# Performance work log

Hardware: AMD Instinct MI355X
Metric: run time of the kernel (lower is better)

## Reference

```python
import jax, jax.numpy as jnp
import numpy as np
from jax import lax

N = 16384      # total nodes (NG graphs x PER nodes)
PER = 512      # nodes per graph
NG = 32        # number of graphs
E = 262144     # edges (avg degree 16)
NEG = jnp.float32(-1e30)


def gcn_conv(x, W, b, src, dst, em, n):
    # PyG GCNConv: h = xW; add *remaining* self-loops; symmetric norm; aggregate at dst; + bias
    h = x @ W
    w = em.astype(x.dtype)
    selfw = jax.ops.segment_sum(jnp.where((src == dst) & em, 1.0, 0.0), dst, num_segments=n)
    has_self = (selfw > 0).astype(x.dtype)
    deg = jax.ops.segment_sum(w, dst, num_segments=n) + (1.0 - has_self)
    dinv = lax.rsqrt(deg)
    norm = dinv[src] * dinv[dst] * w                      # [E]
    agg = jax.ops.segment_sum(norm[:, None] * h[src], dst, num_segments=n)
    return agg + ((1.0 - has_self) / deg)[:, None] * h + b


def edge_pool(x, src, dst, em, nvalid, Pw, Pb, n):
    # PyG EdgePooling with softmax edge scores, add_to_edge_score=0.1, eval-mode dropout (identity)
    e = src.shape[0]
    raw = (jnp.concatenate([x[src], x[dst]], axis=1) @ Pw)[:, 0] + Pb[0]
    # softmax over edges grouped by target node
    logits = jnp.where(em, raw, NEG)
    mx = jax.ops.segment_max(logits, dst, num_segments=n)
    ex = jnp.where(em, jnp.exp(raw - mx[dst]), 0.0)
    den = jax.ops.segment_sum(ex, dst, num_segments=n)
    score = jnp.where(em, ex / jnp.maximum(den[dst], 1e-16), 0.0) + 0.1
    # greedy sequential edge contraction in descending score order (matches PyG __merge_edges__)
    key = lax.stop_gradient(jnp.where(em, score, NEG))
    order = jnp.argsort(-key)

    def step(marked, sdm):
        s, d, mk = sdm
        ok = mk & ~marked[s] & ~marked[d]
        m1 = marked.at[s].set(marked[s] | ok)
        m2 = m1.at[d].set(m1[d] | ok)
        return m2, ok

    _, ch_sorted = lax.scan(step, ~nvalid, (src[order], dst[order], em[order]))
    chosen = jnp.zeros(e, bool).at[order].set(ch_sorted)

    rep = jnp.minimum(src, dst)
    oth = jnp.maximum(src, dst)
    SEN = n  # out-of-range index -> dropped scatter
    cluster = jnp.arange(n, dtype=src.dtype).at[jnp.where(chosen, oth, SEN)].set(rep, mode='drop')
    node_score = jnp.ones(n, x.dtype).at[jnp.where(chosen, rep, SEN)].set(score, mode='drop')
    absorbed = jnp.zeros(n, bool).at[jnp.where(chosen & (src != dst), oth, SEN)].set(True, mode='drop')
    new_valid = nvalid & ~absorbed
    # new_x[c] = (sum of x over cluster) * edge score (1 for unmatched nodes)
    new_x = jax.ops.segment_sum(x, cluster, num_segments=n) * node_score[:, None]
    new_x = new_x * new_valid[:, None].astype(x.dtype)
    # remap + coalesce edges (dedupe); padding kept via mask
    ns, nd = cluster[src], cluster[dst]
    ekey = jnp.where(em, ns * n + nd, n * n)
    eo = jnp.argsort(ekey)
    ks = ekey[eo]
    dup = jnp.concatenate([jnp.zeros(1, bool), ks[1:] == ks[:-1]])
    return new_x, ns[eo], nd[eo], (ks < n * n) & ~dup, new_valid


def _forward(x, W1, b1, W2, b2, W3, b3, P1w, P1b, P2w, P2b, P3w, P3b,
             L1w, L1b, L2w, L2b, L3w, L3b, edge_index, batch):
    n = x.shape[0]
    src, dst = edge_index[0], edge_index[1]
    em = jnp.ones(src.shape[0], bool)
    nv = jnp.ones(n, bool)
    h = gcn_conv(x, W1, b1, src, dst, em, n)
    h, src, dst, em, nv = edge_pool(h, src, dst, em, nv, P1w, P1b, n)
    h = jax.nn.relu(h)
    h = gcn_conv(h, W2, b2, src, dst, em, n)
    h, src, dst, em, nv = edge_pool(h, src, dst, em, nv, P2w, P2b, n)
    h = jax.nn.relu(h)
    h = gcn_conv(h, W3, b3, src, dst, em, n)
    h, src, dst, em, nv = edge_pool(h, src, dst, em, nv, P3w, P3b, n)
    h = jax.nn.relu(h)
    beff = jnp.where(nv, batch, NG)                       # invalid nodes -> dummy segment
    g = jax.ops.segment_max(h, beff, num_segments=NG + 1)[:NG]
    z = jax.nn.relu(g @ L1w + L1b)
    z = jax.nn.relu(z @ L2w + L2b)
    z = jax.nn.relu(z @ L3w + L3b)
    return jax.nn.softmax(z, axis=-1)


def _lin(k, fi, fo):
    w = jax.random.normal(k, (fi, fo), jnp.float32) * (1.0 / np.sqrt(fi))
    return w, jnp.zeros((fo,), jnp.float32)


def setup_inputs() -> dict:
    key = jax.random.key(0)
    ks = jax.random.split(key, 16)
    x = jax.random.normal(ks[0], (N, 107), jnp.float32)
    src = jax.random.randint(ks[1], (E,), 0, N, dtype=jnp.int32)
    dst = (src // PER) * PER + jax.random.randint(ks[2], (E,), 0, PER, dtype=jnp.int32)
    edge_index = jnp.stack([src, dst])
    batch = jnp.arange(N, dtype=jnp.int32) // PER
    W1, b1 = _lin(ks[3], 107, 200)
    W2, b2 = _lin(ks[4], 200, 400)
    W3, b3 = _lin(ks[5], 400, 600)
    P1w, P1b = _lin(ks[6], 400, 1)
    P2w, P2b = _lin(ks[7], 800, 1)
    P3w, P3b = _lin(ks[8], 1200, 1)
    L1w, L1b = _lin(ks[9], 600, 200)
    L2w, L2b = _lin(ks[10], 200, 20)
    L3w, L3b = _lin(ks[11], 20, 4)
    return dict(x=x, edge_index=edge_index, batch=batch,
                W1=W1, b1=b1, W2=W2, b2=b2, W3=W3, b3=b3,
                P1w=P1w, P1b=P1b, P2w=P2w, P2b=P2b, P3w=P3w, P3b=P3b,
                L1w=L1w, L1b=L1b, L2w=L2w, L2b=L2b, L3w=L3w, L3b=L3b)


def reference(x, edge_index, batch, W1, b1, W2, b2, W3, b3,
              P1w, P1b, P2w, P2b, P3w, P3b, L1w, L1b, L2w, L2b, L3w, L3b):
    return _forward(x, W1, b1, W2, b2, W3, b3, P1w, P1b, P2w, P2b, P3w, P3b,
                    L1w, L1b, L2w, L2b, L3w, L3b, edge_index, batch)
```

## Files before the change

### kernel.cpp

```cpp
#include <hip/hip_runtime.h>

#define NN 16384
#define PERG 512
#define NGR 32
#define NE 262144
#define GSEG 9216

typedef unsigned long long u64;

__device__ __forceinline__ unsigned encf(float f){
  unsigned u = __float_as_uint(f);
  return (u & 0x80000000u) ? ~u : (u | 0x80000000u);
}
__device__ __forceinline__ float decf(unsigned e){
  unsigned u = (e & 0x80000000u) ? (e ^ 0x80000000u) : ~e;
  return __uint_as_float(u);
}

__global__ void k_padx(const float* __restrict__ x, float* __restrict__ xp){
  int i = blockIdx.x*256 + threadIdx.x;
  if (i < NN*112){ int r = i/112, c = i-r*112; xp[i] = (c<107) ? x[r*107+c] : 0.f; }
}
__global__ void k_padw(const float* __restrict__ Wsrc, float* __restrict__ Wdst,
                       int Ksrc, int Kdst, int N){
  int i = blockIdx.x*256 + threadIdx.x;
  if (i < Kdst*N){ int r = i/N, c = i-r*N; Wdst[i] = (r<Ksrc) ? Wsrc[r*N+c] : 0.f; }
}

__global__ __launch_bounds__(256) void k_bucket(const int* __restrict__ ei, int* __restrict__ gcount,
    int* __restrict__ bsrc, int* __restrict__ bdst, int* __restrict__ bem, int* __restrict__ beid){
  __shared__ int cnt[NGR];
  __shared__ int base[NGR];
  int t = threadIdx.x;
  if (t < NGR) cnt[t] = 0;
  __syncthreads();
  int e = blockIdx.x*256 + t;
  int s=0,d=0,g=0,r=0;
  bool ok = (e < NE);
  if (ok){ s = ei[e]; d = ei[NE+e]; g = s >> 9; r = atomicAdd(&cnt[g],1); }
  __syncthreads();
  if (t < NGR) base[t] = atomicAdd(&gcount[t], cnt[t]);
  __syncthreads();
  if (ok){
    int pos = g*GSEG + base[g] + r;
    bsrc[pos]=s; bdst[pos]=d; bem[pos]=1; beid[pos]=e;
  }
}
__global__ void k_init_nodes(int* __restrict__ valid){
  int i = blockIdx.x*256 + threadIdx.x;
  if (i < NN) valid[i]=1;
}

__global__ __launch_bounds__(256) void k_mm(const float* __restrict__ A, const float* __restrict__ W,
                                            float* __restrict__ C, int KP, int N){
  __shared__ float As[16][132];
  __shared__ float Ws[16][68];
  int col0 = blockIdx.x*64, row0 = blockIdx.y*128;
  int t = threadIdx.x;
  int tx = t & 15, ty = t >> 4;
  int ar = t >> 1;
  int ak = (t & 1) * 8;
  int wk = t >> 4;
  int wn = (t & 15) * 4;
  int wc = col0 + wn;

  float acc[8][4];
#pragma unroll
  for (int i=0;i<8;i++)
#pragma unroll
    for (int j=0;j<4;j++) acc[i][j]=0.f;

  const float* Arow = A + (size_t)(row0+ar)*KP;

  for (int k0=0; k0<KP; k0+=16){
    float4 a0 = *(const float4*)&Arow[k0 + ak];
    float4 a1 = *(const float4*)&Arow[k0 + ak + 4];
    float4 w0;
    const float* wp = &W[(size_t)(k0+wk)*N + wc];
    if (wc+3 < N) w0 = *(const float4*)wp;
    else { w0.x=(wc<N)?wp[0]:0.f; w0.y=(wc+1<N)?wp[1]:0.f; w0.z=(wc+2<N)?wp[2]:0.f; w0.w=0.f; }
    __syncthreads();
    As[ak+0][ar]=a0.x; As[ak+1][ar]=a0.y; As[ak+2][ar]=a0.z; As[ak+3][ar]=a0.w;
    As[ak+4][ar]=a1.x; As[ak+5][ar]=a1.y; As[ak+6][ar]=a1.z; As[ak+7][ar]=a1.w;
    *(float4*)&Ws[wk][wn] = w0;
    __syncthreads();
#pragma unroll
    for (int kk=0;kk<16;kk++){
      float4 A0 = *(const float4*)&As[kk][ty*8];
      float4 A1 = *(const float4*)&As[kk][ty*8+4];
      float4 B0 = *(const float4*)&Ws[kk][tx*4];
      float a[8] = {A0.x,A0.y,A0.z,A0.w,A1.x,A1.y,A1.z,A1.w};
      float b[4] = {B0.x,B0.y,B0.z,B0.w};
#pragma unroll
      for (int i=0;i<8;i++)
#pragma unroll
        for (int j=0;j<4;j++) acc[i][j] += a[i]*b[j];
    }
  }

#pragma unroll
  for (int i=0;i<8;i++){
    int r = row0 + ty*8 + i;
    int cc = col0 + tx*4;
    if (cc+3 < N){
      float4 v = {acc[i][0],acc[i][1],acc[i][2],acc[i][3]};
      *(float4*)&C[(size_t)r*N+cc] = v;
    } else {
#pragma unroll
      for (int j=0;j<4;j++) if (cc+j<N) C[(size_t)r*N+cc+j] = acc[i][j];
    }
  }
}

__global__ __launch_bounds__(1024) void k_prep(const int* __restrict__ bsrc, const int* __restrict__ bdst,
    const int* __restrict__ bem, const int* __restrict__ gcount,
    int* __restrict__ row_s, int* __restrict__ row_e, int* __restrict__ elist,
    float* __restrict__ dinv, float* __restrict__ selfco){
  int g = blockIdx.x, t = threadIdx.x;
  __shared__ int cnt_l[PERG];
  __shared__ int scn[PERG];
  __shared__ int cur[PERG];
  __shared__ unsigned char hs_l[PERG];
  if (t<PERG){ cnt_l[t]=0; hs_l[t]=0; }
  __syncthreads();
  int nE = min(gcount[g], GSEG); int base = g*GSEG;
  for (int k=t;k<nE;k+=1024){
    if (bem[base+k]){
      int d = bdst[base+k]&511;
      atomicAdd(&cnt_l[d],1);
      if (bsrc[base+k]==bdst[base+k]) hs_l[d]=1;
    }
  }
  __syncthreads();
  if (t<PERG) scn[t]=cnt_l[t];
  __syncthreads();
  for (int off=1; off<PERG; off<<=1){
    int v = (t<PERG && t>=off) ? scn[t-off] : 0;
    __syncthreads();
    if (t<PERG) scn[t]+=v;
    __syncthreads();
  }
  if (t<PERG){
    int excl = scn[t]-cnt_l[t];
    row_s[g*PERG+t] = base+excl;
    row_e[g*PERG+t] = base+scn[t];
    cur[t] = excl;
    float deg = (float)cnt_l[t] + (hs_l[t]?0.f:1.f);
    dinv[g*PERG+t]   = rsqrtf(deg);
    selfco[g*PERG+t] = hs_l[t]?0.f:(1.f/deg);
  }
  __syncthreads();
  for (int k=t;k<nE;k+=1024){
    if (bem[base+k]){
      int d = bdst[base+k]&511;
      elist[base + atomicAdd(&cur[d],1)] = bsrc[base+k];
    }
  }
}

template<int FO>
__global__ __launch_bounds__(256) void k_aggab(const float* __restrict__ h, const int* __restrict__ row_s,
    const int* __restrict__ row_e, const int* __restrict__ elist,
    const float* __restrict__ dinv, const float* __restrict__ selfco, const float* __restrict__ bias,
    const float* __restrict__ Pw, float* __restrict__ y, float* __restrict__ aval, float* __restrict__ bval){
  constexpr int Q = (FO+63)/64;
  int lane = threadIdx.x & 63;
  int nblk = (blockIdx.x & 7)*512 + (blockIdx.x >> 3);
  int i = nblk*4 + (threadIdx.x>>6);
  float acc[Q];
#pragma unroll
  for (int q=0;q<Q;q++) acc[q]=0.f;
  int s0 = row_s[i], s1 = row_e[i];
  float di = dinv[i];
  for (int p=s0; p<s1; p++){
    int s = elist[p];
    float nr = di * dinv[s];
    const float* hrow = h + (size_t)s*FO;
#pragma unroll
    for (int q=0;q<Q;q++){ int c=lane+q*64; if (c<FO) acc[q] += nr*hrow[c]; }
  }
  float sc = selfco[i];
  const float* hi = h + (size_t)i*FO;
  float* yi = y + (size_t)i*FO;
  float sa=0.f, sb=0.f;
#pragma unroll
  for (int q=0;q<Q;q++){
    int c = lane+q*64;
    if (c<FO){
      float v = acc[q] + sc*hi[c] + bias[c];
      yi[c] = v;
      sa += v*Pw[c];
      sb += v*Pw[FO+c];
    }
  }
  for (int o=32;o;o>>=1){ sa += __shfl_xor(sa,o); sb += __shfl_xor(sb,o); }
  if (lane==0){ aval[i]=sa; bval[i]=sb; }
}

#define NEPT 9
__global__ __launch_bounds__(1024) void k_pool(const int* __restrict__ gcount,
    int* __restrict__ bsrc, int* __restrict__ bdst, int* __restrict__ bem, const int* __restrict__ beid,
    const float* __restrict__ aval, const float* __restrict__ bval, const float* __restrict__ Pb,
    float* __restrict__ nscore, int* __restrict__ partner, int* __restrict__ valid, int* __restrict__ table){
  extern __shared__ u64 dynL[];
  u64* list = dynL;
  unsigned* sdL = (unsigned*)(dynL + GSEG);
  __shared__ unsigned mx[PERG];
  __shared__ float den[PERG];
  __shared__ u64 best[PERG];
  __shared__ unsigned char marked[PERG];
  __shared__ unsigned short clus[PERG];
  __shared__ int cntA;
  int g = blockIdx.x, t = threadIdx.x;
  int nE = min(gcount[g], GSEG), base = g*GSEG;
  if (t<PERG){
    mx[t]=0u; den[t]=0.f; best[t]=0ull;
    marked[t] = valid[(g<<9)+t] ? 0 : 1;
    clus[t] = (unsigned short)t;
    nscore[(g<<9)+t] = 1.f;
    partner[(g<<9)+t] = -1;
  }
  if (t==0) cntA = 0;
  __syncthreads();

  int sL[NEPT], dL[NEPT];
  float rawv[NEPT];
  unsigned em = 0u;
#pragma unroll
  for (int j=0;j<NEPT;j++){
    sL[j]=0; dL[j]=0; rawv[j]=0.f;
    int k = t + j*1024;
    if (k < nE && bem[base+k]){
      sL[j] = bsrc[base+k]&511; dL[j] = bdst[base+k]&511;
      rawv[j] = aval[(g<<9)+sL[j]] + bval[(g<<9)+dL[j]] + Pb[0];
      em |= (1u<<j);
      atomicMax(&mx[dL[j]], encf(rawv[j]));
    }
  }
  __syncthreads();
  float exv[NEPT];
#pragma unroll
  for (int j=0;j<NEPT;j++){
    exv[j]=0.f;
    if (em & (1u<<j)){
      exv[j] = expf(rawv[j] - decf(mx[dL[j]]));
      atomicAdd(&den[dL[j]], exv[j]);
    }
  }
  __syncthreads();
#pragma unroll
  for (int j=0;j<NEPT;j++){
    if (em & (1u<<j)){
      int k = t + j*1024;
      float sc = exv[j]/fmaxf(den[dL[j]],1e-16f) + 0.1f;
      int s = sL[j], d = dL[j];
      sdL[k] = ((unsigned)s<<9) | (unsigned)d;
      if (!(marked[s]|marked[d])){
        u64 rec = ((u64)__float_as_uint(sc) << 32)
                | ((u64)(0x3FFFFu - (unsigned)beid[base+k]) << 14) | (u64)k;
        list[atomicAdd(&cntA,1)] = rec;
      }
    }
  }
  __syncthreads();

  while (true){
    int cn = cntA;
    if (cn == 0) break;
    for (int i=t;i<cn;i+=1024){
      u64 rec = list[i];
      unsigned sd = sdL[(unsigned)(rec & 0x3FFFu)];
      int s = sd>>9, d = sd&511;
      atomicMax(&best[s], rec);
      if (d != s) atomicMax(&best[d], rec);
    }
    __syncthreads();
    for (int i=t;i<cn;i+=1024){
      u64 rec = list[i];
      unsigned sd = sdL[(unsigned)(rec & 0x3FFFu)];
      int s = sd>>9, d = sd&511;
      if (best[s]==rec && (s==d || best[d]==rec)){
        unsigned sb = (unsigned)(rec >> 32);
        if (s == d){
          marked[s] = 1;
          nscore[(g<<9)+s] = __uint_as_float(sb);
        } else {
          int rep = min(s,d), oth = max(s,d);
          clus[oth] = (unsigned short)rep;
          nscore[(g<<9)+rep] = __uint_as_float(sb);
          valid[(g<<9)+oth] = 0;
          partner[(g<<9)+rep] = (g<<9)+oth;
          marked[s] = 1; marked[d] = 1;
        }
      }
    }
    __syncthreads();
    u64 keep[NEPT]; unsigned km = 0u;
#pragma unroll
    for (int j=0;j<NEPT;j++){
      keep[j] = 0ull;
      int i = t + j*1024;
      if (i < cn){
        u64 rec = list[i];
        unsigned sd = sdL[(unsigned)(rec & 0x3FFFu)];
        int s = sd>>9, d = sd&511;
        if (!(marked[s]|marked[d])){ keep[j]=rec; km |= (1u<<j); }
      }
    }
    __syncthreads();
    if (t==0) cntA = 0;
    if (t<PERG) best[t] = 0ull;
    __syncthreads();
#pragma unroll
    for (int j=0;j<NEPT;j++){
      if (km & (1u<<j)) list[atomicAdd(&cntA,1)] = keep[j];
    }
    __syncthreads();
  }
  __syncthreads();

#pragma unroll
  for (int j=0;j<NEPT;j++){
    if (em & (1u<<j)){
      int k = t + j*1024;
      int ns = clus[sL[j]], nd = clus[dL[j]];
      sL[j]=ns; dL[j]=nd;
      bsrc[base+k] = (g<<9)+ns; bdst[base+k] = (g<<9)+nd;
      table[(g<<18) | (ns<<9) | nd] = 0x7FFFFFFF;
    }
  }
  __syncthreads();
#pragma unroll
  for (int j=0;j<NEPT;j++){
    if (em & (1u<<j)){
      int k = t + j*1024;
      atomicMin(&table[(g<<18) | (sL[j]<<9) | dL[j]], base+k);
    }
  }
  __syncthreads();
#pragma unroll
  for (int j=0;j<NEPT;j++){
    if (em & (1u<<j)){
      int k = t + j*1024;
      if (table[(g<<18) | (sL[j]<<9) | dL[j]] != base+k) bem[base+k] = 0;
    }
  }
}

template<int FO, int FOP>
__global__ __launch_bounds__(256) void k_newx(const float* __restrict__ y, const int* __restrict__ partner,
    const float* __restrict__ nscore, const int* __restrict__ valid, float* __restrict__ out){
  constexpr int Q = (FOP+63)/64;
  int lane = threadIdx.x & 63;
  int nblk = (blockIdx.x & 7)*512 + (blockIdx.x >> 3);
  int i = nblk*4 + (threadIdx.x>>6);
  int v = valid[i];
  float ns = nscore[i];
  int p = partner[i];
  const float* yi = y + (size_t)i*FO;
  const float* yp = (p>=0) ? (y + (size_t)p*FO) : yi;
  float* oi = out + (size_t)i*FOP;
#pragma unroll
  for (int q=0;q<Q;q++){
    int c = lane + q*64;
    if (c<FO){
      float val = yi[c];
      if (p>=0) val += yp[c];
      val *= ns;
      oi[c] = v ? fmaxf(val,0.f) : 0.f;
    } else if (c<FOP){
      oi[c] = 0.f;
    }
  }
}

__global__ __launch_bounds__(256) void k_gmax(const float* __restrict__ x, const int* __restrict__ valid,
                                              float* __restrict__ part){
  int g = blockIdx.x >> 3, rp = blockIdx.x & 7;
  __shared__ int lv[64];
  int r0 = rp*64;
  if (threadIdx.x < 64) lv[threadIdx.x] = valid[g*PERG + r0 + threadIdx.x];
  __syncthreads();
  const float* base = x + ((size_t)g*PERG + r0)*600;
  for (int c=threadIdx.x; c<600; c+=256){
    float m = -1e30f;
    for (int r=0;r<64;r++)
      if (lv[r]) m = fmaxf(m, base[(size_t)r*600+c]);
    part[(size_t)(g*8+rp)*600 + c] = m;
  }
}
__global__ __launch_bounds__(256) void k_head(const float* __restrict__ part,
    const float* __restrict__ L1w, const float* __restrict__ L1b,
    const float* __restrict__ L2w, const float* __restrict__ L2b,
    const float* __restrict__ L3w, const float* __restrict__ L3b, float* __restrict__ out){
  int g = blockIdx.x, t = threadIdx.x;
  __shared__ float gg[600];
  __shared__ float z1[200];
  __shared__ float z2[20];
  __shared__ float z3[4];
  for (int c=t;c<600;c+=256){
    float m = -1e30f;
#pragma unroll
    for (int rp=0;rp<8;rp++) m = fmaxf(m, part[(size_t)(g*8+rp)*600 + c]);
    gg[c] = m;
  }
  __syncthreads();
  if (t<200){
    float s = L1b[t];
#pragma unroll 4
    for (int k=0;k<600;k++) s += gg[k]*L1w[k*200+t];
    z1[t] = fmaxf(s,0.f);
  }
  __syncthreads();
  if (t<20){
    float s = L2b[t];
#pragma unroll 4
    for (int k=0;k<200;k++) s += z1[k]*L2w[k*20+t];
    z2[t] = fmaxf(s,0.f);
  }
  __syncthreads();
  if (t<4){
    float s = L3b[t];
    for (int k=0;k<20;k++) s += z2[k]*L3w[k*4+t];
    z3[t] = fmaxf(s,0.f);
  }
  __syncthreads();
  if (t==0){
    float m = fmaxf(fmaxf(z3[0],z3[1]), fmaxf(z3[2],z3[3]));
    float e0=expf(z3[0]-m), e1=expf(z3[1]-m), e2=expf(z3[2]-m), e3=expf(z3[3]-m);
    float s = e0+e1+e2+e3;
    out[g*4+0]=e0/s; out[g*4+1]=e1/s; out[g*4+2]=e2/s; out[g*4+3]=e3/s;
  }
}

struct WsPtrs {
  float *A, *B, *x0p, *W1p, *W2p;
  int *bsrc, *bdst, *bem, *beid;
  int *elist, *row_s, *row_e;
  float *dinv, *selfco, *aval, *bval;
  float *nscore; int *partner; int *valid;
  int *gcount;
  float *gbuf;
};

extern "C" void kernel_launch(void* const* d_in, const int* in_sizes, int n_in,
                              void* d_out, int out_size, void* d_ws, size_t ws_size,
                              hipStream_t stream){
  const float* x0  = (const float*)d_in[0];
  const int*   ei  = (const int*)  d_in[1];
  const float* W1  = (const float*)d_in[3];  const float* b1  = (const float*)d_in[4];
  const float* W2  = (const float*)d_in[5];  const float* b2  = (const float*)d_in[6];
  const float* W3  = (const float*)d_in[7];  const float* b3  = (const float*)d_in[8];
  const float* P1w = (const float*)d_in[9];  const float* P1b = (const float*)d_in[10];
  const float* P2w = (const float*)d_in[11]; const float* P2b = (const float*)d_in[12];
  const float* P3w = (const float*)d_in[13]; const float* P3b = (const float*)d_in[14];
  const float* L1w = (const float*)d_in[15]; const float* L1b = (const float*)d_in[16];
  const float* L2w = (const float*)d_in[17]; const float* L2b = (const float*)d_in[18];
  const float* L3w = (const float*)d_in[19]; const float* L3b = (const float*)d_in[20];
  float* out = (float*)d_out;

  char* w = (char*)d_ws;
  size_t off = 0;
  auto alloc = [&](size_t bytes)->void*{
    void* p = w + off;
    off += bytes;
    off = (off + 255) & ~(size_t)255;
    return p;
  };
  WsPtrs P;
  P.A     = (float*)alloc((size_t)NN*600*4);
  P.B     = (float*)alloc((size_t)NN*600*4);
  P.x0p   = (float*)alloc((size_t)NN*112*4);
  P.W1p   = (float*)alloc((size_t)112*200*4);
  P.W2p   = (float*)alloc((size_t)208*400*4);
  P.bsrc  = (int*)  alloc((size_t)NGR*GSEG*4);
  P.bdst  = (int*)  alloc((size_t)NGR*GSEG*4);
  P.bem   = (int*)  alloc((size_t)NGR*GSEG*4);
  P.beid  = (int*)  alloc((size_t)NGR*GSEG*4);
  P.elist = (int*)  alloc((size_t)NGR*GSEG*4);
  P.row_s = (int*)  alloc((size_t)NN*4);
  P.row_e = (int*)  alloc((size_t)NN*4);
  P.dinv   = (float*)alloc((size_t)NN*4);
  P.selfco = (float*)alloc((size_t)NN*4);
  P.aval   = (float*)alloc((size_t)NN*4);
  P.bval   = (float*)alloc((size_t)NN*4);
  P.nscore = (float*)alloc((size_t)NN*4);
  P.partner= (int*)  alloc((size_t)NN*4);
  P.valid  = (int*)  alloc((size_t)NN*4);
  P.gcount = (int*)  alloc((size_t)NGR*4);
  P.gbuf   = (float*)alloc((size_t)NGR*8*600*4);
  (void)ws_size; (void)in_sizes; (void)n_in; (void)out_size;

  const int NG4 = NN/4;
  const int POOL_LDS = GSEG*8 + GSEG*4;

  k_padx<<<(NN*112+255)/256,256,0,stream>>>(x0, P.x0p);
  k_padw<<<(112*200+255)/256,256,0,stream>>>(W1, P.W1p, 107, 112, 200);
  k_padw<<<(208*400+255)/256,256,0,stream>>>(W2, P.W2p, 200, 208, 400);
  hipMemsetAsync(P.gcount, 0, NGR*sizeof(int), stream);
  k_bucket<<<NE/256,256,0,stream>>>(ei, P.gcount, P.bsrc, P.bdst, P.bem, P.beid);
  k_init_nodes<<<NN/256,256,0,stream>>>(P.valid);

  { dim3 gmm(4,128); k_mm<<<gmm,256,0,stream>>>(P.x0p, P.W1p, P.A, 112, 200); }
  k_prep<<<NGR,1024,0,stream>>>(P.bsrc,P.bdst,P.bem,P.gcount,P.row_s,P.row_e,P.elist,P.dinv,P.selfco);
  k_aggab<200><<<NG4,256,0,stream>>>(P.A,P.row_s,P.row_e,P.elist,P.dinv,P.selfco,b1,P1w,P.B,P.aval,P.bval);
  k_pool<<<NGR,1024,POOL_LDS,stream>>>(P.gcount,P.bsrc,P.bdst,P.bem,P.beid,
                                P.aval,P.bval,P1b,P.nscore,P.partner,P.valid,(int*)P.A);
  k_newx<200,208><<<NG4,256,0,stream>>>(P.B,P.partner,P.nscore,P.valid,P.A);

  { dim3 gmm(7,128); k_mm<<<gmm,256,0,stream>>>(P.A, P.W2p, P.B, 208, 400); }
  k_prep<<<NGR,1024,0,stream>>>(P.bsrc,P.bdst,P.bem,P.gcount,P.row_s,P.row_e,P.elist,P.dinv,P.selfco);
  k_aggab<400><<<NG4,256,0,stream>>>(P.B,P.row_s,P.row_e,P.elist,P.dinv,P.selfco,b2,P2w,P.A,P.aval,P.bval);
  k_pool<<<NGR,1024,POOL_LDS,stream>>>(P.gcount,P.bsrc,P.bdst,P.bem,P.beid,
                                P.aval,P.bval,P2b,P.nscore,P.partner,P.valid,(int*)P.B);
  k_newx<400,400><<<NG4,256,0,stream>>>(P.A,P.partner,P.nscore,P.valid,P.B);

  { dim3 gmm(10,128); k_mm<<<gmm,256,0,stream>>>(P.B, W3, P.A, 400, 600); }
  k_prep<<<NGR,1024,0,stream>>>(P.bsrc,P.bdst,P.bem,P.gcount,P.row_s,P.row_e,P.elist,P.dinv,P.selfco);
  k_aggab<600><<<NG4,256,0,stream>>>(P.A,P.row_s,P.row_e,P.elist,P.dinv,P.selfco,b3,P3w,P.B,P.aval,P.bval);
  k_pool<<<NGR,1024,POOL_LDS,stream>>>(P.gcount,P.bsrc,P.bdst,P.bem,P.beid,
                                P.aval,P.bval,P3b,P.nscore,P.partner,P.valid,(int*)P.A);
  k_newx<600,600><<<NG4,256,0,stream>>>(P.B,P.partner,P.nscore,P.valid,P.A);

  k_gmax<<<NGR*8,256,0,stream>>>(P.A, P.valid, P.gbuf);
  k_head<<<NGR,256,0,stream>>>(P.gbuf, L1w, L1b, L2w, L2b, L3w, L3b, out);
}
```

Measured before the change: 957.9 us.

## Rework edge pooling with CSR softmax, warp-aggregated appends, and LDS hash dedup

The per-destination softmax max and denominator are now computed by one thread per node walking the CSR rows built by k_prep, with aval and bval staged in LDS. This replaces the shared atomicMax and atomicAdd passes. Appends to the candidate list use ballot-based warp aggregation, so each wave issues one atomic instead of one per lane. Duplicate-edge removal now uses an open-addressing hash table in LDS that reuses the list buffer, instead of a large global table with three global passes. The trade-offs are serial per-node loops, hash probing cost, and reliance on the CSR being consistent with the current edge mask.

New measurement: 945.1 us. No clear change (-1.3%).

```diff
diff --git a/kernel.cpp b/kernel.cpp
--- a/kernel.cpp
+++ b/kernel.cpp
@@ -5,17 +5,9 @@
 #define NGR 32
 #define NE 262144
 #define GSEG 9216
+#define HSIZE 16384
 
 typedef unsigned long long u64;
-
-__device__ __forceinline__ unsigned encf(float f){
-  unsigned u = __float_as_uint(f);
-  return (u & 0x80000000u) ? ~u : (u | 0x80000000u);
-}
-__device__ __forceinline__ float decf(unsigned e){
-  unsigned u = (e & 0x80000000u) ? (e ^ 0x80000000u) : ~e;
-  return __uint_as_float(u);
-}
 
 __global__ void k_padx(const float* __restrict__ x, float* __restrict__ xp){
   int i = blockIdx.x*256 + threadIdx.x;
@@ -200,21 +192,25 @@
 #define NEPT 9
 __global__ __launch_bounds__(1024) void k_pool(const int* __restrict__ gcount,
     int* __restrict__ bsrc, int* __restrict__ bdst, int* __restrict__ bem, const int* __restrict__ beid,
+    const int* __restrict__ row_s, const int* __restrict__ row_e, const int* __restrict__ elist,
     const float* __restrict__ aval, const float* __restrict__ bval, const float* __restrict__ Pb,
-    float* __restrict__ nscore, int* __restrict__ partner, int* __restrict__ valid, int* __restrict__ table){
+    float* __restrict__ nscore, int* __restrict__ partner, int* __restrict__ valid){
   extern __shared__ u64 dynL[];
   u64* list = dynL;
   unsigned* sdL = (unsigned*)(dynL + GSEG);
-  __shared__ unsigned mx[PERG];
-  __shared__ float den[PERG];
+  unsigned* hashT = (unsigned*)dynL;
+  __shared__ float avalL[PERG], bvalL[PERG], mxL[PERG], denL[PERG];
   __shared__ u64 best[PERG];
   __shared__ unsigned char marked[PERG];
   __shared__ unsigned short clus[PERG];
   __shared__ int cntA;
   int g = blockIdx.x, t = threadIdx.x;
+  int lane = t & 63;
   int nE = min(gcount[g], GSEG), base = g*GSEG;
   if (t<PERG){
-    mx[t]=0u; den[t]=0.f; best[t]=0ull;
+    avalL[t] = aval[(g<<9)+t];
+    bvalL[t] = bval[(g<<9)+t];
+    best[t]=0ull;
     marked[t] = valid[(g<<9)+t] ? 0 : 1;
     clus[t] = (unsigned short)t;
     nscore[(g<<9)+t] = 1.f;
@@ -223,43 +219,46 @@
   if (t==0) cntA = 0;
   __syncthreads();
 
+  float pb = Pb[0];
+  if (t<PERG){
+    int p0 = row_s[(g<<9)+t], p1 = row_e[(g<<9)+t];
+    float bv = bvalL[t];
+    float m = -1e30f;
+    for (int p=p0;p<p1;p++) m = fmaxf(m, avalL[elist[p]&511] + bv + pb);
+    float dn = 0.f;
+    for (int p=p0;p<p1;p++) dn += expf(avalL[elist[p]&511] + bv + pb - m);
+    mxL[t] = m;
+    denL[t] = fmaxf(dn, 1e-16f);
+  }
+  __syncthreads();
+
   int sL[NEPT], dL[NEPT];
-  float rawv[NEPT];
   unsigned em = 0u;
 #pragma unroll
   for (int j=0;j<NEPT;j++){
-    sL[j]=0; dL[j]=0; rawv[j]=0.f;
+    sL[j]=0; dL[j]=0;
     int k = t + j*1024;
+    bool want = false; u64 rec = 0ull;
     if (k < nE && bem[base+k]){
-      sL[j] = bsrc[base+k]&511; dL[j] = bdst[base+k]&511;
-      rawv[j] = aval[(g<<9)+sL[j]] + bval[(g<<9)+dL[j]] + Pb[0];
-      em |= (1u<<j);
-      atomicMax(&mx[dL[j]], encf(rawv[j]));
-    }
-  }
-  __syncthreads();
-  float exv[NEPT];
-#pragma unroll
-  for (int j=0;j<NEPT;j++){
-    exv[j]=0.f;
-    if (em & (1u<<j)){
-      exv[j] = expf(rawv[j] - decf(mx[dL[j]]));
-      atomicAdd(&den[dL[j]], exv[j]);
-    }
-  }
-  __syncthreads();
-#pragma unroll
-  for (int j=0;j<NEPT;j++){
-    if (em & (1u<<j)){
-      int k = t + j*1024;
-      float sc = exv[j]/fmaxf(den[dL[j]],1e-16f) + 0.1f;
-      int s = sL[j], d = dL[j];
+      int s = bsrc[base+k]&511, d = bdst[base+k]&511;
+      sL[j]=s; dL[j]=d; em |= (1u<<j);
       sdL[k] = ((unsigned)s<<9) | (unsigned)d;
       if (!(marked[s]|marked[d])){
-        u64 rec = ((u64)__float_as_uint(sc) << 32)
-                | ((u64)(0x3FFFFu - (unsigned)beid[base+k]) << 14) | (u64)k;
-        list[atomicAdd(&cntA,1)] = rec;
+        float raw = avalL[s] + bvalL[d] + pb;
+        float sc = expf(raw - mxL[d]) / denL[d] + 0.1f;
+        rec = ((u64)__float_as_uint(sc) << 32)
+            | ((u64)(0x3FFFFu - (unsigned)beid[base+k]) << 14) | (u64)k;
+        want = true;
       }
+    }
+    unsigned long long mask = __ballot(want);
+    if (want){
+      int leader = __builtin_ctzll(mask);
+      int rank = __popcll(mask & ((1ull<<lane)-1ull));
+      int bs = 0;
+      if (lane == leader) bs = atomicAdd(&cntA, __popcll(mask));
+      bs = __shfl(bs, leader);
+      list[bs + rank] = rec;
     }
   }
   __syncthreads();
@@ -313,12 +312,23 @@
     __syncthreads();
 #pragma unroll
     for (int j=0;j<NEPT;j++){
-      if (km & (1u<<j)) list[atomicAdd(&cntA,1)] = keep[j];
-    }
-    __syncthreads();
-  }
-  __syncthreads();
-
+      bool want = (km & (1u<<j)) != 0u;
+      unsigned long long mask = __ballot(want);
+      if (want){
+        int leader = __builtin_ctzll(mask);
+        int rank = __popcll(mask & ((1ull<<lane)-1ull));
+        int bs = 0;
+        if (lane == leader) bs = atomicAdd(&cntA, __popcll(mask));
+        bs = __shfl(bs, leader);
+        list[bs + rank] = keep[j];
+      }
+    }
+    __syncthreads();
+  }
+  __syncthreads();
+
+  for (int i=t;i<HSIZE;i+=1024) hashT[i] = 0xFFFFFFFFu;
+  __syncthreads();
 #pragma unroll
   for (int j=0;j<NEPT;j++){
     if (em & (1u<<j)){
@@ -326,7 +336,18 @@
       int ns = clus[sL[j]], nd = clus[dL[j]];
       sL[j]=ns; dL[j]=nd;
       bsrc[base+k] = (g<<9)+ns; bdst[base+k] = (g<<9)+nd;
-      table[(g<<18) | (ns<<9) | nd] = 0x7FFFFFFF;
+      unsigned key = ((unsigned)ns<<9) | (unsigned)nd;
+      unsigned ent = (key<<14) | (unsigned)k;
+      unsigned hh = (key*2654435761u) >> 18;
+      for (;;){
+        unsigned cur = hashT[hh];
+        if (cur == 0xFFFFFFFFu){
+          cur = atomicCAS(&hashT[hh], 0xFFFFFFFFu, ent);
+          if (cur == 0xFFFFFFFFu) break;
+        }
+        if ((cur>>14) == key){ atomicMin(&hashT[hh], ent); break; }
+        hh = (hh+1) & (HSIZE-1);
+      }
     }
   }
   __syncthreads();
@@ -334,15 +355,16 @@
   for (int j=0;j<NEPT;j++){
     if (em & (1u<<j)){
       int k = t + j*1024;
-      atomicMin(&table[(g<<18) | (sL[j]<<9) | dL[j]], base+k);
-    }
-  }
-  __syncthreads();
-#pragma unroll
-  for (int j=0;j<NEPT;j++){
-    if (em & (1u<<j)){
-      int k = t + j*1024;
-      if (table[(g<<18) | (sL[j]<<9) | dL[j]] != base+k) bem[base+k] = 0;
+      unsigned key = ((unsigned)sL[j]<<9) | (unsigned)dL[j];
+      unsigned hh = (key*2654435761u) >> 18;
+      for (;;){
+        unsigned cur = hashT[hh];
+        if (cur != 0xFFFFFFFFu && (cur>>14) == key){
+          if ((int)(cur & 0x3FFFu) != k) bem[base+k] = 0;
+          break;
+        }
+        hh = (hh+1) & (HSIZE-1);
+      }
     }
   }
 }
@@ -505,21 +527,24 @@
   k_prep<<<NGR,1024,0,stream>>>(P.bsrc,P.bdst,P.bem,P.gcount,P.row_s,P.row_e,P.elist,P.dinv,P.selfco);
   k_aggab<200><<<NG4,256,0,stream>>>(P.A,P.row_s,P.row_e,P.elist,P.dinv,P.selfco,b1,P1w,P.B,P.aval,P.bval);
   k_pool<<<NGR,1024,POOL_LDS,stream>>>(P.gcount,P.bsrc,P.bdst,P.bem,P.beid,
-                                P.aval,P.bval,P1b,P.nscore,P.partner,P.valid,(int*)P.A);
+                                P.row_s,P.row_e,P.elist,
+                                P.aval,P.bval,P1b,P.nscore,P.partner,P.valid);
   k_newx<200,208><<<NG4,256,0,stream>>>(P.B,P.partner,P.nscore,P.valid,P.A);
 
   { dim3 gmm(7,128); k_mm<<<gmm,256,0,stream>>>(P.A, P.W2p, P.B, 208, 400); }
   k_prep<<<NGR,1024,0,stream>>>(P.bsrc,P.bdst,P.bem,P.gcount,P.row_s,P.row_e,P.elist,P.dinv,P.selfco);
   k_aggab<400><<<NG4,256,0,stream>>>(P.B,P.row_s,P.row_e,P.elist,P.dinv,P.selfco,b2,P2w,P.A,P.aval,P.bval);
   k_pool<<<NGR,1024,POOL_LDS,stream>>>(P.gcount,P.bsrc,P.bdst,P.bem,P.beid,
-                                P.aval,P.bval,P2b,P.nscore,P.partner,P.valid,(int*)P.B);
+                                P.row_s,P.row_e,P.elist,
+                                P.aval,P.bval,P2b,P.nscore,P.partner,P.valid);
   k_newx<400,400><<<NG4,256,0,stream>>>(P.A,P.partner,P.nscore,P.valid,P.B);
 
   { dim3 gmm(10,128); k_mm<<<gmm,256,0,stream>>>(P.B, W3, P.A, 400, 600); }
   k_prep<<<NGR,1024,0,stream>>>(P.bsrc,P.bdst,P.bem,P.gcount,P.row_s,P.row_e,P.elist,P.dinv,P.selfco);
   k_aggab<600><<<NG4,256,0,stream>>>(P.A,P.row_s,P.row_e,P.elist,P.dinv,P.selfco,b3,P3w,P.B,P.aval,P.bval);
   k_pool<<<NGR,1024,POOL_LDS,stream>>>(P.gcount,P.bsrc,P.bdst,P.bem,P.beid,
-                                P.aval,P.bval,P3b,P.nscore,P.partner,P.valid,(int*)P.A);
+                                P.row_s,P.row_e,P.elist,
+                                P.aval,P.bval,P3b,P.nscore,P.partner,P.valid);
   k_newx<600,600><<<NG4,256,0,stream>>>(P.B,P.partner,P.nscore,P.valid,P.A);
 
   k_gmax<<<NGR*8,256,0,stream>>>(P.A, P.valid, P.gbuf);
```
